# Optimization experiments

Measured on AMD Instinct MI355X. Metric: run time of the kernel, lower is better.

## Reference

```python
import jax, jax.numpy as jnp
import numpy as np

HIDDEN = 128
GLOBAL_HIDDEN = 128
STATE_DIM = 8
FEATURE = HIDDEN + GLOBAL_HIDDEN + STATE_DIM  # 264, as in SympleAgent.feature_size
NUM_OPS = 30
NUM_INTERNAL_OPS = 5
N_NODES = 400000


def _ffn(x, W1, b1, W2, b2):
    # FFN(in, hidden, out, n_layers=1): Linear -> ReLU -> Linear
    return jax.nn.relu(x @ W1 + b1) @ W2 + b2


def setup_inputs() -> dict:
    key = jax.random.key(0)
    ks = jax.random.split(key, 20)
    s = 0.02

    def lin(k, fan_in, fan_out):
        k1, k2 = jax.random.split(k)
        return (jax.random.normal(k1, (fan_in, fan_out), jnp.float32) * s,
                jax.random.normal(k2, (fan_out,), jnp.float32) * s)

    W_hl1, b_hl1 = lin(ks[0], FEATURE, HIDDEN)
    W_hl2, b_hl2 = lin(ks[1], HIDDEN, 4)            # high_level_actor -> 4
    W_in1, b_in1 = lin(ks[2], FEATURE, HIDDEN)
    W_in2, b_in2 = lin(ks[3], HIDDEN, NUM_INTERNAL_OPS)  # internal_actor
    W_ex1, b_ex1 = lin(ks[4], FEATURE, HIDDEN)
    W_ex2, b_ex2 = lin(ks[5], HIDDEN, NUM_OPS)      # actor (external ops)
    W_tp1, b_tp1 = lin(ks[6], FEATURE, HIDDEN)
    W_tp2, b_tp2 = lin(ks[7], HIDDEN, 1)            # teleport_ffn -> 1 per node

    node_hidden = jax.random.normal(ks[8], (N_NODES, HIDDEN), jnp.float32)
    h_glob = jax.random.normal(ks[9], (1, GLOBAL_HIDDEN), jnp.float32)
    state_tensor = jax.random.normal(ks[10], (1, STATE_DIM), jnp.float32)
    validity_mask = jnp.ones((1, NUM_OPS), jnp.float32)

    return {
        "node_hidden": node_hidden, "h_glob": h_glob,
        "state_tensor": state_tensor, "validity_mask": validity_mask,
        "W_hl1": W_hl1, "b_hl1": b_hl1, "W_hl2": W_hl2, "b_hl2": b_hl2,
        "W_in1": W_in1, "b_in1": b_in1, "W_in2": W_in2, "b_in2": b_in2,
        "W_ex1": W_ex1, "b_ex1": b_ex1, "W_ex2": W_ex2, "b_ex2": b_ex2,
        "W_tp1": W_tp1, "b_tp1": b_tp1, "W_tp2": W_tp2, "b_tp2": b_tp2,
    }


def reference(node_hidden, h_glob, state_tensor, validity_mask,
              W_hl1, b_hl1, W_hl2, b_hl2,
              W_in1, b_in1, W_in2, b_in2,
              W_ex1, b_ex1, W_ex2, b_ex2,
              W_tp1, b_tp1, W_tp2, b_tp2):
    # --- get_policy_logits for current node (coord -> node 0) ---
    cur = node_hidden[0:1]                                   # [1, H]
    feats = jnp.concatenate([cur, h_glob, state_tensor], -1)  # [1, FEATURE]
    l_high = _ffn(feats, W_hl1, b_hl1, W_hl2, b_hl2)          # [1, 4]
    l_internal = _ffn(feats, W_in1, b_in1, W_in2, b_in2)      # [1, 5]
    l_ext = _ffn(feats, W_ex1, b_ex1, W_ex2, b_ex2) + jnp.log(validity_mask)  # [1, NUM_OPS]

    # --- apply_teleport_ffn: features over all n_nodes ---
    n = node_hidden.shape[0]
    hg = jnp.broadcast_to(h_glob, (n, h_glob.shape[-1]))      # h_glob[-1].repeat(n,1)
    st = jnp.broadcast_to(state_tensor, (n, state_tensor.shape[-1]))
    tp_feats = jnp.concatenate([hg, node_hidden, st], -1)     # [n, FEATURE]
    l_teleport = _ffn(tp_feats, W_tp1, b_tp1, W_tp2, b_tp2).T  # [1, n]

    # concatenate all heads along the logit axis: [1, 4 + 5 + NUM_OPS + n]
    return jnp.concatenate([l_high, l_internal, l_ext, l_teleport], axis=-1)
```

## Files before the change

### kernel.cpp

```cpp
#include <hip/hip_runtime.h>
#include <hip/hip_bf16.h>
#include <stdint.h>

typedef __attribute__((ext_vector_type(8))) short short8;
typedef __bf16 bf16x8 __attribute__((ext_vector_type(8)));
typedef __attribute__((ext_vector_type(4))) float f32x4;

#define HID 128
#define NTILES 8
#define KSTEPS 4

#define WS_C_F    8192
#define WS_W2_F   8320
#define WS_B2_F   8448

#define TP_BLOCKS   256
#define TP_WAVES    5
#define TP_THREADS  (TP_WAVES * 64)
#define TOTAL_TP_WAVES (TP_BLOCKS * TP_WAVES)

#define SLOT_BYTES    8192
#define WEIGHTS_BYTES 33792
#define SMEM_BYTES    (WEIGHTS_BYTES + TP_WAVES * 3 * SLOT_BYTES)

__global__ void prep_kernel(const float* __restrict__ node_hidden,
                            const float* __restrict__ h_glob,
                            const float* __restrict__ state,
                            const float* __restrict__ validity,
                            const float* __restrict__ W_hl1, const float* __restrict__ b_hl1,
                            const float* __restrict__ W_hl2, const float* __restrict__ b_hl2,
                            const float* __restrict__ W_in1, const float* __restrict__ b_in1,
                            const float* __restrict__ W_in2, const float* __restrict__ b_in2,
                            const float* __restrict__ W_ex1, const float* __restrict__ b_ex1,
                            const float* __restrict__ W_ex2, const float* __restrict__ b_ex2,
                            const float* __restrict__ W_tp1, const float* __restrict__ b_tp1,
                            const float* __restrict__ W_tp2, const float* __restrict__ b_tp2,
                            float* __restrict__ out, float* __restrict__ ws)
{
    const int tid = threadIdx.x;
    const int b = blockIdx.x;

    if (b < 3) {
        __shared__ float feats[264];
        __shared__ float hpart[4][128];
        __shared__ float hidden[128];
        const float* W1 = (b == 0) ? W_hl1 : (b == 1 ? W_in1 : W_ex1);
        const float* b1 = (b == 0) ? b_hl1 : (b == 1 ? b_in1 : b_ex1);
        const float* W2 = (b == 0) ? W_hl2 : (b == 1 ? W_in2 : W_ex2);
        const float* b2 = (b == 0) ? b_hl2 : (b == 1 ? b_in2 : b_ex2);
        const int od    = (b == 0) ? 4 : (b == 1 ? 5 : 30);
        const int obase = (b == 0) ? 0 : (b == 1 ? 4 : 9);

        if (tid < 264) {
            float v;
            if (tid < 128)      v = node_hidden[tid];
            else if (tid < 256) v = h_glob[tid - 128];
            else                v = state[tid - 256];
            feats[tid] = v;
        }
        __syncthreads();
        {
            const int j = tid & 127, q = tid >> 7;
            float s = 0.f;
            for (int i = q * 66; i < q * 66 + 66; ++i) s += feats[i] * W1[i * 128 + j];
            hpart[q][j] = s;
        }
        __syncthreads();
        if (tid < 128) {
            float h = b1[tid] + hpart[0][tid] + hpart[1][tid] + hpart[2][tid] + hpart[3][tid];
            hidden[tid] = fmaxf(h, 0.f);
        }
        __syncthreads();
        if (tid < od) {
            float o = b2[tid];
            for (int i = 0; i < 128; ++i) o += hidden[i] * W2[i * od + tid];
            if (b == 2) o += logf(validity[tid]);
            out[obase + tid] = o;
        }
    } else if (b == 3) {
        __shared__ float cpart[4][128];
        {
            const int j = tid & 127, q = tid >> 7;
            float s = 0.f;
            for (int i = q * 32; i < q * 32 + 32; ++i) s += h_glob[i] * W_tp1[i * HID + j];
            if (q == 3)
                for (int i = 0; i < 8; ++i) s += state[i] * W_tp1[(256 + i) * HID + j];
            cpart[q][j] = s;
        }
        __syncthreads();
        if (tid < 128) {
            ws[WS_C_F  + tid] = b_tp1[tid] + cpart[0][tid] + cpart[1][tid]
                                           + cpart[2][tid] + cpart[3][tid];
            ws[WS_W2_F + tid] = W_tp2[tid];
            if (tid == 0) ws[WS_B2_F] = b_tp2[0];
        }
    } else {
        short* afrag = (short*)ws;
        const int part = b - 4;
        for (int idx = part * 1024 + tid; idx < part * 1024 + 1024; idx += 512) {
            const int k = idx >> 7, nn = idx & 127;
            const int t = nn >> 4, cc = nn & 15;
            const int s = k >> 5, rr = k & 31;
            const int g = rr >> 3, j = rr & 7;
            const int lane = cc + (g << 4);
            afrag[(((t * KSTEPS + s) * 64 + lane) << 3) + j] =
                (short)__builtin_bit_cast(unsigned short, (__bf16)W_tp1[(128 + k) * HID + nn]);
        }
    }
}

__launch_bounds__(TP_THREADS)
__global__ void teleport_kernel(const float* __restrict__ node_hidden,
                                const float* __restrict__ ws,
                                float* __restrict__ out,
                                int n)
{
    __shared__ __align__(16) unsigned char smem[SMEM_BYTES];
    const int tid = threadIdx.x;

    {
        const int4* wsv = (const int4*)ws;
        int4* sv = (int4*)smem;
        for (int i = tid; i < 2112; i += TP_THREADS) sv[i] = wsv[i];
    }
    const float bias2 = ws[WS_B2_F];
    __syncthreads();

    const short* afrag  = (const short*)smem;
    const float* c_all  = (const float*)(smem + 32768);
    const float* w2_all = (const float*)(smem + 33280);

    const int lane = tid & 63;
    const int wave = tid >> 6;
    const int m  = lane & 15;
    const int g  = lane >> 4;
    const unsigned mx = (unsigned)(m & 7);
    const unsigned mrow = (unsigned)m * 512;

    unsigned char* p0 = smem + WEIGHTS_BYTES + wave * 3 * SLOT_BYTES;
    unsigned char* p1 = p0 + SLOT_BYTES;
    unsigned char* p2 = p1 + SLOT_BYTES;

    const int nChunks = (n + 15) >> 4;
    const int gw = blockIdx.x * TP_WAVES + wave;
    const int c0 = (int)(((long long)gw * nChunks) / TOTAL_TP_WAVES);
    const int c1 = (int)(((long long)(gw + 1) * nChunks) / TOTAL_TP_WAVES);

#define STAGE(slot_, c_)                                                         \
    {                                                                            \
        _Pragma("unroll")                                                        \
        for (int k_ = 0; k_ < 8; ++k_) {                                         \
            const int row_ = 2 * k_ + (lane >> 5);                               \
            const int grow_ = min((c_) * 16 + row_, n - 1);                      \
            const unsigned su_ = ((unsigned)(lane & 31)) ^ ((unsigned)(row_ & 7));\
            const unsigned char* src_ = (const unsigned char*)node_hidden        \
                                        + (size_t)grow_ * 512 + (su_ << 4);      \
            __builtin_amdgcn_global_load_lds(                                    \
                (const __attribute__((address_space(1))) unsigned int*)src_,     \
                (__attribute__((address_space(3))) unsigned int*)(slot_ + k_ * 1024), \
                16, 0, 0);                                                       \
        }                                                                        \
    }

    if (c0 < c1) {
        STAGE(p0, c0);
        if (c0 + 1 < c1) STAGE(p1, c0 + 1);
        if (c0 + 2 < c1) STAGE(p2, c0 + 2);

        for (int c = c0; c < c1; ++c) {
            if (c + 3 <= c1) {
                if (c >= c0 + 3) { asm volatile("s_waitcnt vmcnt(19)" ::: "memory"); }
                else             { asm volatile("s_waitcnt vmcnt(16)" ::: "memory"); }
            } else if (c + 2 == c1) {
                asm volatile("s_waitcnt vmcnt(8)" ::: "memory");
            } else {
                asm volatile("s_waitcnt vmcnt(0)" ::: "memory");
            }

            bf16x8 nd[KSTEPS];
            #pragma unroll
            for (int s = 0; s < KSTEPS; ++s) {
                const unsigned u0 = (((unsigned)(s * 8 + g * 2))     ^ mx) << 4;
                const unsigned u1 = (((unsigned)(s * 8 + g * 2 + 1)) ^ mx) << 4;
                const float4 fa = *(const float4*)(p0 + mrow + u0);
                const float4 fb = *(const float4*)(p0 + mrow + u1);
                bf16x8 a;
                a[0] = (__bf16)fa.x; a[1] = (__bf16)fa.y; a[2] = (__bf16)fa.z; a[3] = (__bf16)fa.w;
                a[4] = (__bf16)fb.x; a[5] = (__bf16)fb.y; a[6] = (__bf16)fb.z; a[7] = (__bf16)fb.w;
                nd[s] = a;
            }
            __builtin_amdgcn_sched_barrier(0);
            if (c + 3 < c1) STAGE(p0, c + 3);

            float sr = 0.f;
            #pragma unroll
            for (int t = 0; t < NTILES; ++t) {
                f32x4 acc = (f32x4){0.f, 0.f, 0.f, 0.f};
                #pragma unroll
                for (int s = 0; s < KSTEPS; ++s) {
                    const short8 wv = *(const short8*)&afrag[(((t * KSTEPS + s) * 64 + lane) << 3)];
                    const bf16x8 wf = __builtin_bit_cast(bf16x8, wv);
                    acc = __builtin_amdgcn_mfma_f32_16x16x32_bf16(wf, nd[s], acc, 0, 0, 0);
                }
                const float4 c4 = *(const float4*)(c_all  + t * 16 + g * 4);
                const float4 w4 = *(const float4*)(w2_all + t * 16 + g * 4);
                float h0 = acc[0] + c4.x, h1 = acc[1] + c4.y;
                float h2 = acc[2] + c4.z, h3 = acc[3] + c4.w;
                h0 = h0 > 0.f ? h0 : 0.f;  h1 = h1 > 0.f ? h1 : 0.f;
                h2 = h2 > 0.f ? h2 : 0.f;  h3 = h3 > 0.f ? h3 : 0.f;
                sr += h0 * w4.x + h1 * w4.y + h2 * w4.z + h3 * w4.w;
            }

            sr += __shfl_xor(sr, 16, 64);
            sr += __shfl_xor(sr, 32, 64);

            if (lane < 16) {
                const int o = c * 16 + lane;
                if (o < n) out[o] = sr + bias2;
            }

            unsigned char* tmp = p0; p0 = p1; p1 = p2; p2 = tmp;
        }
    }
#undef STAGE
}

extern "C" void kernel_launch(void* const* d_in, const int* in_sizes, int n_in,
                              void* d_out, int out_size, void* d_ws, size_t ws_size,
                              hipStream_t stream) {
    const float* node_hidden = (const float*)d_in[0];
    const float* h_glob      = (const float*)d_in[1];
    const float* state       = (const float*)d_in[2];
    const float* validity    = (const float*)d_in[3];
    const float* W_hl1 = (const float*)d_in[4];  const float* b_hl1 = (const float*)d_in[5];
    const float* W_hl2 = (const float*)d_in[6];  const float* b_hl2 = (const float*)d_in[7];
    const float* W_in1 = (const float*)d_in[8];  const float* b_in1 = (const float*)d_in[9];
    const float* W_in2 = (const float*)d_in[10]; const float* b_in2 = (const float*)d_in[11];
    const float* W_ex1 = (const float*)d_in[12]; const float* b_ex1 = (const float*)d_in[13];
    const float* W_ex2 = (const float*)d_in[14]; const float* b_ex2 = (const float*)d_in[15];
    const float* W_tp1 = (const float*)d_in[16]; const float* b_tp1 = (const float*)d_in[17];
    const float* W_tp2 = (const float*)d_in[18]; const float* b_tp2 = (const float*)d_in[19];

    float* out = (float*)d_out;
    float* ws  = (float*)d_ws;
    const int n = in_sizes[0] / HID;

    prep_kernel<<<20, 512, 0, stream>>>(node_hidden, h_glob, state, validity,
                                        W_hl1, b_hl1, W_hl2, b_hl2,
                                        W_in1, b_in1, W_in2, b_in2,
                                        W_ex1, b_ex1, W_ex2, b_ex2,
                                        W_tp1, b_tp1, W_tp2, b_tp2,
                                        out, ws);
    teleport_kernel<<<TP_BLOCKS, TP_THREADS, 0, stream>>>(node_hidden, ws, out + 39, n);
}
```

Baseline: 52.20 us.

## Use 8 waves with double-buffered staging and register-resident bias/W2

Raises waves per block from 5 to 8 and cuts each wave's prefetch ring from three LDS slots to two, so more waves fit in a similar LDS budget and rebalances the per-wave chunk split. The layer-1 bias and layer-2 weights now sit in registers loaded once, removing two LDS reads per tile per chunk. The vmcnt wait thresholds are rewritten for the shallower pipeline. Each wave has less prefetch depth and register pressure rises from the 64 extra floats, in exchange for more latency hiding from the extra waves.

```diff
diff --git a/kernel.cpp b/kernel.cpp
--- a/kernel.cpp
+++ b/kernel.cpp
@@ -15,13 +15,13 @@
 #define WS_B2_F   8448
 
 #define TP_BLOCKS   256
-#define TP_WAVES    5
+#define TP_WAVES    8
 #define TP_THREADS  (TP_WAVES * 64)
 #define TOTAL_TP_WAVES (TP_BLOCKS * TP_WAVES)
 
 #define SLOT_BYTES    8192
-#define WEIGHTS_BYTES 33792
-#define SMEM_BYTES    (WEIGHTS_BYTES + TP_WAVES * 3 * SLOT_BYTES)
+#define AFRAG_BYTES   32768
+#define SMEM_BYTES    (AFRAG_BYTES + TP_WAVES * 2 * SLOT_BYTES)
 
 __global__ void prep_kernel(const float* __restrict__ node_hidden,
                             const float* __restrict__ h_glob,
@@ -118,18 +118,6 @@
     __shared__ __align__(16) unsigned char smem[SMEM_BYTES];
     const int tid = threadIdx.x;
 
-    {
-        const int4* wsv = (const int4*)ws;
-        int4* sv = (int4*)smem;
-        for (int i = tid; i < 2112; i += TP_THREADS) sv[i] = wsv[i];
-    }
-    const float bias2 = ws[WS_B2_F];
-    __syncthreads();
-
-    const short* afrag  = (const short*)smem;
-    const float* c_all  = (const float*)(smem + 32768);
-    const float* w2_all = (const float*)(smem + 33280);
-
     const int lane = tid & 63;
     const int wave = tid >> 6;
     const int m  = lane & 15;
@@ -137,9 +125,24 @@
     const unsigned mx = (unsigned)(m & 7);
     const unsigned mrow = (unsigned)m * 512;
 
-    unsigned char* p0 = smem + WEIGHTS_BYTES + wave * 3 * SLOT_BYTES;
+    {
+        const int4* wsv = (const int4*)ws;
+        int4* sv = (int4*)smem;
+        for (int i = tid; i < 2048; i += TP_THREADS) sv[i] = wsv[i];
+    }
+    f32x4 cR[NTILES], wR[NTILES];
+    #pragma unroll
+    for (int t = 0; t < NTILES; ++t) {
+        cR[t] = *(const f32x4*)(ws + WS_C_F  + t * 16 + g * 4);
+        wR[t] = *(const f32x4*)(ws + WS_W2_F + t * 16 + g * 4);
+    }
+    const float bias2 = ws[WS_B2_F];
+    __syncthreads();
+
+    const short* afrag = (const short*)smem;
+
+    unsigned char* p0 = smem + AFRAG_BYTES + wave * 2 * SLOT_BYTES;
     unsigned char* p1 = p0 + SLOT_BYTES;
-    unsigned char* p2 = p1 + SLOT_BYTES;
 
     const int nChunks = (n + 15) >> 4;
     const int gw = blockIdx.x * TP_WAVES + wave;
@@ -165,17 +168,12 @@
     if (c0 < c1) {
         STAGE(p0, c0);
         if (c0 + 1 < c1) STAGE(p1, c0 + 1);
-        if (c0 + 2 < c1) STAGE(p2, c0 + 2);
 
         for (int c = c0; c < c1; ++c) {
-            if (c + 3 <= c1) {
-                if (c >= c0 + 3) { asm volatile("s_waitcnt vmcnt(19)" ::: "memory"); }
-                else             { asm volatile("s_waitcnt vmcnt(16)" ::: "memory"); }
-            } else if (c + 2 == c1) {
-                asm volatile("s_waitcnt vmcnt(8)" ::: "memory");
-            } else {
-                asm volatile("s_waitcnt vmcnt(0)" ::: "memory");
-            }
+            if (c == c1 - 1)      { asm volatile("s_waitcnt vmcnt(0)"  ::: "memory"); }
+            else if (c == c0)     { asm volatile("s_waitcnt vmcnt(8)"  ::: "memory"); }
+            else if (c == c0 + 1) { asm volatile("s_waitcnt vmcnt(9)"  ::: "memory"); }
+            else                  { asm volatile("s_waitcnt vmcnt(10)" ::: "memory"); }
 
             bf16x8 nd[KSTEPS];
             #pragma unroll
@@ -190,7 +188,7 @@
                 nd[s] = a;
             }
             __builtin_amdgcn_sched_barrier(0);
-            if (c + 3 < c1) STAGE(p0, c + 3);
+            if (c + 2 < c1) STAGE(p0, c + 2);
 
             float sr = 0.f;
             #pragma unroll
@@ -202,13 +200,11 @@
                     const bf16x8 wf = __builtin_bit_cast(bf16x8, wv);
                     acc = __builtin_amdgcn_mfma_f32_16x16x32_bf16(wf, nd[s], acc, 0, 0, 0);
                 }
-                const float4 c4 = *(const float4*)(c_all  + t * 16 + g * 4);
-                const float4 w4 = *(const float4*)(w2_all + t * 16 + g * 4);
-                float h0 = acc[0] + c4.x, h1 = acc[1] + c4.y;
-                float h2 = acc[2] + c4.z, h3 = acc[3] + c4.w;
+                float h0 = acc[0] + cR[t][0], h1 = acc[1] + cR[t][1];
+                float h2 = acc[2] + cR[t][2], h3 = acc[3] + cR[t][3];
                 h0 = h0 > 0.f ? h0 : 0.f;  h1 = h1 > 0.f ? h1 : 0.f;
                 h2 = h2 > 0.f ? h2 : 0.f;  h3 = h3 > 0.f ? h3 : 0.f;
-                sr += h0 * w4.x + h1 * w4.y + h2 * w4.z + h3 * w4.w;
+                sr += h0 * wR[t][0] + h1 * wR[t][1] + h2 * wR[t][2] + h3 * wR[t][3];
             }
 
             sr += __shfl_xor(sr, 16, 64);
@@ -219,7 +215,7 @@
                 if (o < n) out[o] = sr + bias2;
             }
 
-            unsigned char* tmp = p0; p0 = p1; p1 = p2; p2 = tmp;
+            unsigned char* tmp = p0; p0 = p1; p1 = tmp;
         }
     }
 #undef STAGE
```

Result: faster. 48.50 us (-7.1%).
